# Kernel tuning notes

Measured on AMD Instinct MI355X. Metric: run time of the kernel, lower is better.

The kernel has to match this reference:

```python
import jax, jax.numpy as jnp
import numpy as np

D_MODEL = 1024
NUM_HEADS = 16
HEAD_DIM = D_MODEL // NUM_HEADS


def setup_inputs() -> dict:
    key = jax.random.key(0)
    ks = jax.random.split(key, 9)
    B, S = 2, 2048
    s = 1.0 / np.sqrt(D_MODEL)
    inp = {
        "x": jax.random.normal(ks[0], (B, S, D_MODEL), dtype=jnp.float32),
        "Wq": jax.random.normal(ks[1], (D_MODEL, D_MODEL), dtype=jnp.float32) * s,
        "bq": jnp.zeros((D_MODEL,), dtype=jnp.float32),
        "Wk": jax.random.normal(ks[2], (D_MODEL, D_MODEL), dtype=jnp.float32) * s,
        "bk": jnp.zeros((D_MODEL,), dtype=jnp.float32),
        "Wv": jax.random.normal(ks[3], (D_MODEL, D_MODEL), dtype=jnp.float32) * s,
        "bv": jnp.zeros((D_MODEL,), dtype=jnp.float32),
        "Wo": jax.random.normal(ks[4], (D_MODEL, D_MODEL), dtype=jnp.float32) * s,
        "bo": jnpp if False else jnp.zeros((D_MODEL,), dtype=jnp.float32),
    }
    return inp


def reference(x, Wq, bq, Wk, bk, Wv, bv, Wo, bo):
    B, S, D = x.shape
    H, hd = NUM_HEADS, HEAD_DIM
    # QKV projections (Linear: x @ W^T + b), split into heads -> [B,H,S,hd]
    q = (x @ Wq.T + bq).reshape(B, S, H, hd).transpose(0, 2, 1, 3)
    k = (x @ Wk.T + bk).reshape(B, S, H, hd).transpose(0, 2, 1, 3)
    v = (x @ Wv.T + bv).reshape(B, S, H, hd).transpose(0, 2, 1, 3)
    # scores [B,H,S,S]
    scores = jnp.einsum('bhqd,bhkd->bhqk', q, k) / jnp.sqrt(jnp.float32(hd))
    p = jax.nn.softmax(scores, axis=-1)
    out = jnp.einsum('bhqk,bhkd->bhqd', p, v)  # [B,H,S,hd]
    out = out.transpose(0, 2, 1, 3).reshape(B, S, D)
    return out @ Wo.T + bo
```

## Files before the change

### kernel.cpp

```cpp
#include <hip/hip_runtime.h>
#include <hip/hip_bf16.h>
#include <math.h>

typedef __bf16 bf16;
typedef unsigned short u16;
typedef __bf16 bf16x8 __attribute__((ext_vector_type(8)));
typedef __bf16 bf16x4 __attribute__((ext_vector_type(4)));
typedef short  s16x4  __attribute__((ext_vector_type(4)));
typedef float  f32x4  __attribute__((ext_vector_type(4)));

#define D_MODEL 1024
#define NHEAD   16
#define HD      64
#define BATCH   2
#define SEQ     2048
#define MTOT    (BATCH*SEQ)

#define EXPSCALE 0.18033688011116016f

__device__ __forceinline__ void async16(const void* g, void* l) {
    __builtin_amdgcn_global_load_lds(
        (__attribute__((address_space(1))) unsigned int*)g,
        (__attribute__((address_space(3))) unsigned int*)l,
        16, 0, 0);
}

__device__ __forceinline__ f32x4 mfma16(s16x4 a, s16x4 b, f32x4 c) {
    return __builtin_amdgcn_mfma_f32_16x16x16bf16_1k(a, b, c, 0, 0, 0);
}

__global__ __launch_bounds__(256) void cast_kernel(
    const float* __restrict__ x,
    const float* __restrict__ wq, const float* __restrict__ wk,
    const float* __restrict__ wv, const float* __restrict__ wo,
    bf16* __restrict__ xb, bf16* __restrict__ wqb, bf16* __restrict__ wkb,
    bf16* __restrict__ wvb, bf16* __restrict__ wob)
{
    const int z = blockIdx.y;
    const float* src;
    bf16* dst;
    int n;
    if (z == 0)      { src = x;  dst = xb;  n = MTOT * D_MODEL; }
    else if (z == 1) { src = wq; dst = wqb; n = D_MODEL * D_MODEL; }
    else if (z == 2) { src = wk; dst = wkb; n = D_MODEL * D_MODEL; }
    else if (z == 3) { src = wv; dst = wvb; n = D_MODEL * D_MODEL; }
    else             { src = wo; dst = wob; n = D_MODEL * D_MODEL; }

    int i = (blockIdx.x * 256 + threadIdx.x) * 8;
    if (i >= n) return;
    float4 a = *(const float4*)(src + i);
    float4 b = *(const float4*)(src + i + 4);
    bf16x8 o;
    o[0] = (bf16)a.x; o[1] = (bf16)a.y; o[2] = (bf16)a.z; o[3] = (bf16)a.w;
    o[4] = (bf16)b.x; o[5] = (bf16)b.y; o[6] = (bf16)b.z; o[7] = (bf16)b.w;
    *(bf16x8*)(dst + i) = o;
}

__device__ __forceinline__ void gemm_core(const bf16* __restrict__ A,
                                          const bf16* __restrict__ W,
                                          int m0, int n0,
                                          f32x4 acc[4][4],
                                          u16* lA, u16* lB)
{
    const int tid  = threadIdx.x;
    const int lane = tid & 63;
    const int wave = tid >> 6;
    const int wr   = wave >> 1;
    const int wc   = wave & 1;
    const int fr   = lane & 15;
    const int quad = lane >> 4;

    #pragma unroll
    for (int mi = 0; mi < 4; ++mi)
        #pragma unroll
        for (int ni = 0; ni < 4; ++ni)
            #pragma unroll
            for (int e = 0; e < 4; ++e)
                acc[mi][ni][e] = 0.0f;

    const int row = tid >> 3;
    const int ca  = ((tid & 7) ^ (row & 7)) * 8;
    const bf16* gA[4];
    const bf16* gB[4];
    u16 *sA[4], *sB[4];
    #pragma unroll
    for (int c = 0; c < 4; ++c) {
        int slot = tid + c * 256;
        int r    = row + c * 32;
        gA[c] = A + (size_t)(m0 + r) * 1024 + ca;
        gB[c] = W + (size_t)(n0 + r) * 1024 + ca;
        sA[c] = lA + (size_t)slot * 8;
        sB[c] = lB + (size_t)slot * 8;
    }

    for (int kt = 0; kt < 1024 / 64; ++kt) {
        __syncthreads();
        #pragma unroll
        for (int c = 0; c < 4; ++c) {
            async16(gA[c] + kt * 64, sA[c]);
            async16(gB[c] + kt * 64, sB[c]);
        }
        __syncthreads();

        #pragma unroll
        for (int ks = 0; ks < 2; ++ks) {
            const int sa = ((ks * 4 + quad) ^ (fr & 7)) * 8;
            bf16x8 af[4], bfm[4];
            #pragma unroll
            for (int mi = 0; mi < 4; ++mi)
                af[mi] = *(const bf16x8*)(lA + (wr * 64 + mi * 16 + fr) * 64 + sa);
            #pragma unroll
            for (int ni = 0; ni < 4; ++ni)
                bfm[ni] = *(const bf16x8*)(lB + (wc * 64 + ni * 16 + fr) * 64 + sa);

            #pragma unroll
            for (int mi = 0; mi < 4; ++mi)
                #pragma unroll
                for (int ni = 0; ni < 4; ++ni)
                    acc[mi][ni] = __builtin_amdgcn_mfma_f32_16x16x32_bf16(
                        af[mi], bfm[ni], acc[mi][ni], 0, 0, 0);
        }
    }
}

__global__ __launch_bounds__(256) void qkv_kernel(
    const bf16* __restrict__ x,
    const bf16* __restrict__ Wq, const bf16* __restrict__ Wk, const bf16* __restrict__ Wv,
    const float* __restrict__ bq, const float* __restrict__ bk, const float* __restrict__ bv,
    bf16* __restrict__ Q, bf16* __restrict__ K, bf16* __restrict__ Vt)
{
    __shared__ __align__(16) u16 lA[128 * 64];
    __shared__ __align__(16) u16 lB[128 * 64];

    const int z = blockIdx.z;
    int m0, n0;
    const bf16 *mA, *mB;
    const float* bias;
    if (z == 2) {
        mA = Wv; mB = x; bias = bv;
        m0 = blockIdx.y * 128;
        n0 = blockIdx.x * 128;
    } else {
        mA = x;  mB = (z == 0) ? Wq : Wk; bias = (z == 0) ? bq : bk;
        m0 = blockIdx.x * 128;
        n0 = blockIdx.y * 128;
    }

    f32x4 acc[4][4];
    gemm_core(mA, mB, m0, n0, acc, lA, lB);

    const int lane = threadIdx.x & 63;
    const int wave = threadIdx.x >> 6;
    const int wr = wave >> 1, wc = wave & 1;
    const int col = lane & 15, quad = lane >> 4;

    if (z == 2) {
        #pragma unroll
        for (int mi = 0; mi < 4; ++mi) {
            #pragma unroll
            for (int ni = 0; ni < 4; ++ni) {
                #pragma unroll
                for (int r = 0; r < 4; ++r) {
                    int f = m0 + wr * 64 + mi * 16 + quad * 4 + r;
                    int t = n0 + wc * 64 + ni * 16 + col;
                    float v = acc[mi][ni][r] + bias[f];
                    int b = t >> 11, s = t & 2047;
                    int h = f >> 6,  d = f & 63;
                    Vt[((size_t)(b * NHEAD + h) * HD + d) * SEQ + s] = (bf16)v;
                }
            }
        }
    } else {
        const float qs = (z == 0) ? EXPSCALE : 1.0f;
        bf16* o = (z == 0) ? Q : K;
        #pragma unroll
        for (int mi = 0; mi < 4; ++mi) {
            #pragma unroll
            for (int ni = 0; ni < 4; ++ni) {
                #pragma unroll
                for (int r = 0; r < 4; ++r) {
                    int m = m0 + wr * 64 + mi * 16 + quad * 4 + r;
                    int n = n0 + wc * 64 + ni * 16 + col;
                    float v = (acc[mi][ni][r] + bias[n]) * qs;
                    int b = m >> 11, s = m & 2047;
                    int h = n >> 6,  d = n & 63;
                    o[((size_t)(b * NHEAD + h) * SEQ + s) * HD + d] = (bf16)v;
                }
            }
        }
    }
}

__global__ __launch_bounds__(256, 2) void attn_kernel(
    const bf16* __restrict__ Q, const bf16* __restrict__ K,
    const bf16* __restrict__ Vt, bf16* __restrict__ O)
{
    __shared__ __align__(16) u16 lK[64 * 64];
    __shared__ __align__(16) u16 lV[64 * 64];

    const int tid  = threadIdx.x;
    const int lane = tid & 63;
    const int wave = tid >> 6;
    const int col  = lane & 15;
    const int quad = lane >> 4;
    const int bh   = blockIdx.x;
    const int q0   = blockIdx.y * 128;

    const bf16* Qh = Q  + (size_t)bh * SEQ * HD;
    const bf16* Kh = K  + (size_t)bh * SEQ * HD;
    const bf16* Vh = Vt + (size_t)bh * HD * SEQ;

    bf16x8 qf[2][2];
    #pragma unroll
    for (int qb = 0; qb < 2; ++qb)
        #pragma unroll
        for (int ks = 0; ks < 2; ++ks)
            qf[qb][ks] = *(const bf16x8*)(
                Qh + (size_t)(q0 + wave * 32 + qb * 16 + col) * HD + ks * 32 + quad * 8);

    f32x4 acc_o[2][4];
    #pragma unroll
    for (int qb = 0; qb < 2; ++qb)
        #pragma unroll
        for (int nd = 0; nd < 4; ++nd)
            #pragma unroll
            for (int e = 0; e < 4; ++e) acc_o[qb][nd][e] = 0.0f;
    float rs[2] = {0.0f, 0.0f};
    const f32x4 zero4 = {0.0f, 0.0f, 0.0f, 0.0f};

    const int r0 = tid >> 3;
    const int r1 = r0 + 32;
    const int g0 = (((tid & 7) ^ (r0 & 7))) * 8;
    const int g1 = (((tid & 7) ^ (r1 & 7))) * 8;
    const bf16* gK0 = Kh + (size_t)r0 * HD + g0;
    const bf16* gK1 = Kh + (size_t)r1 * HD + g1;
    const bf16* gV0 = Vh + (size_t)r0 * SEQ + g0;
    const bf16* gV1 = Vh + (size_t)r1 * SEQ + g1;
    u16* sK0 = lK + (size_t)tid * 8;
    u16* sK1 = lK + (size_t)(tid + 256) * 8;
    u16* sV0 = lV + (size_t)tid * 8;
    u16* sV1 = lV + (size_t)(tid + 256) * 8;

    for (int jt = 0; jt < SEQ / 64; ++jt) {
        __syncthreads();
        async16(gK0 + (size_t)jt * 64 * HD, sK0);
        async16(gK1 + (size_t)jt * 64 * HD, sK1);
        async16(gV0 + jt * 64, sV0);
        async16(gV1 + jt * 64, sV1);
        __syncthreads();

        f32x4 sc[2][4];
        #pragma unroll
        for (int nj = 0; nj < 4; ++nj) {
            bf16x8 kf0 = *(const bf16x8*)(
                lK + (nj * 16 + col) * 64 + ((0 + quad) ^ (col & 7)) * 8);
            sc[0][nj] = __builtin_amdgcn_mfma_f32_16x16x32_bf16(kf0, qf[0][0], zero4, 0, 0, 0);
            sc[1][nj] = __builtin_amdgcn_mfma_f32_16x16x32_bf16(kf0, qf[1][0], zero4, 0, 0, 0);
        }
        #pragma unroll
        for (int nj = 0; nj < 4; ++nj) {
            bf16x8 kf1 = *(const bf16x8*)(
                lK + (nj * 16 + col) * 64 + ((4 + quad) ^ (col & 7)) * 8);
            sc[0][nj] = __builtin_amdgcn_mfma_f32_16x16x32_bf16(kf1, qf[0][1], sc[0][nj], 0, 0, 0);
            sc[1][nj] = __builtin_amdgcn_mfma_f32_16x16x32_bf16(kf1, qf[1][1], sc[1][nj], 0, 0, 0);
        }

        s16x4 pb[2][4];
        #pragma unroll
        for (int qb = 0; qb < 2; ++qb) {
            #pragma unroll
            for (int nj = 0; nj < 4; ++nj) {
                float p0 = __builtin_amdgcn_exp2f(sc[qb][nj][0]);
                float p1 = __builtin_amdgcn_exp2f(sc[qb][nj][1]);
                float p2 = __builtin_amdgcn_exp2f(sc[qb][nj][2]);
                float p3 = __builtin_amdgcn_exp2f(sc[qb][nj][3]);
                rs[qb] += (p0 + p1) + (p2 + p3);
                bf16x4 t;
                t[0] = (bf16)p0; t[1] = (bf16)p1; t[2] = (bf16)p2; t[3] = (bf16)p3;
                pb[qb][nj] = __builtin_bit_cast(s16x4, t);
            }
        }

        #pragma unroll
        for (int nj = 0; nj < 4; ++nj) {
            #pragma unroll
            for (int nd = 0; nd < 4; ++nd) {
                int row = nd * 16 + col;
                int jb  = (2 * nj + (quad >> 1)) ^ (row & 7);
                s16x4 vb = *(const s16x4*)(lV + row * 64 + jb * 8 + (quad & 1) * 4);
                acc_o[0][nd] = mfma16(pb[0][nj], vb, acc_o[0][nd]);
                acc_o[1][nd] = mfma16(pb[1][nj], vb, acc_o[1][nd]);
            }
        }
    }

    const int b = bh >> 4, h = bh & 15;
    #pragma unroll
    for (int qb = 0; qb < 2; ++qb) {
        float v = rs[qb];
        v += __shfl_xor(v, 16);
        v += __shfl_xor(v, 32);
        float inv = 1.0f / v;
        float invr[4];
        #pragma unroll
        for (int r = 0; r < 4; ++r)
            invr[r] = __shfl(inv, quad * 4 + r);
        #pragma unroll
        for (int nd = 0; nd < 4; ++nd) {
            #pragma unroll
            for (int r = 0; r < 4; ++r) {
                int srow = q0 + wave * 32 + qb * 16 + quad * 4 + r;
                int d    = nd * 16 + col;
                float o  = acc_o[qb][nd][r] * invr[r];
                O[((size_t)(b * SEQ + srow)) * D_MODEL + h * HD + d] = (bf16)o;
            }
        }
    }
}

__global__ __launch_bounds__(256) void oproj_kernel(
    const bf16* __restrict__ A, const bf16* __restrict__ Wo,
    const float* __restrict__ bo, float* __restrict__ out)
{
    __shared__ __align__(16) u16 lA[128 * 64];
    __shared__ __align__(16) u16 lB[64 * 64];

    const int m0 = blockIdx.x * 128;
    const int n0 = blockIdx.y * 64;

    const int tid  = threadIdx.x;
    const int lane = tid & 63;
    const int wave = tid >> 6;
    const int wr   = wave >> 1;
    const int wc   = wave & 1;
    const int fr   = lane & 15;
    const int quad = lane >> 4;

    f32x4 acc[4][2];
    #pragma unroll
    for (int mi = 0; mi < 4; ++mi)
        #pragma unroll
        for (int ni = 0; ni < 2; ++ni)
            #pragma unroll
            for (int e = 0; e < 4; ++e)
                acc[mi][ni][e] = 0.0f;

    const int row = tid >> 3;
    const int ca  = ((tid & 7) ^ (row & 7)) * 8;
    const bf16* gA[4];
    u16* sA[4];
    #pragma unroll
    for (int c = 0; c < 4; ++c) {
        int slot = tid + c * 256;
        gA[c] = A + (size_t)(m0 + row + c * 32) * 1024 + ca;
        sA[c] = lA + (size_t)slot * 8;
    }
    const bf16* gB[2];
    u16* sB[2];
    #pragma unroll
    for (int c = 0; c < 2; ++c) {
        int slot = tid + c * 256;
        gB[c] = Wo + (size_t)(n0 + row + c * 32) * 1024 + ca;
        sB[c] = lB + (size_t)slot * 8;
    }

    for (int kt = 0; kt < 1024 / 64; ++kt) {
        __syncthreads();
        #pragma unroll
        for (int c = 0; c < 4; ++c) async16(gA[c] + kt * 64, sA[c]);
        #pragma unroll
        for (int c = 0; c < 2; ++c) async16(gB[c] + kt * 64, sB[c]);
        __syncthreads();

        #pragma unroll
        for (int ks = 0; ks < 2; ++ks) {
            const int sa = ((ks * 4 + quad) ^ (fr & 7)) * 8;
            bf16x8 af[4], bfm[2];
            #pragma unroll
            for (int mi = 0; mi < 4; ++mi)
                af[mi] = *(const bf16x8*)(lA + (wr * 64 + mi * 16 + fr) * 64 + sa);
            #pragma unroll
            for (int ni = 0; ni < 2; ++ni)
                bfm[ni] = *(const bf16x8*)(lB + (wc * 32 + ni * 16 + fr) * 64 + sa);

            #pragma unroll
            for (int mi = 0; mi < 4; ++mi)
                #pragma unroll
                for (int ni = 0; ni < 2; ++ni)
                    acc[mi][ni] = __builtin_amdgcn_mfma_f32_16x16x32_bf16(
                        af[mi], bfm[ni], acc[mi][ni], 0, 0, 0);
        }
    }

    const int col = fr;
    #pragma unroll
    for (int mi = 0; mi < 4; ++mi) {
        #pragma unroll
        for (int ni = 0; ni < 2; ++ni) {
            #pragma unroll
            for (int r = 0; r < 4; ++r) {
                int m = m0 + wr * 64 + mi * 16 + quad * 4 + r;
                int n = n0 + wc * 32 + ni * 16 + col;
                out[(size_t)m * D_MODEL + n] = acc[mi][ni][r] + bo[n];
            }
        }
    }
}

extern "C" void kernel_launch(void* const* d_in, const int* in_sizes, int n_in,
                              void* d_out, int out_size, void* d_ws, size_t ws_size,
                              hipStream_t stream)
{
    const float* x  = (const float*)d_in[0];
    const float* Wq = (const float*)d_in[1];
    const float* bq = (const float*)d_in[2];
    const float* Wk = (const float*)d_in[3];
    const float* bk = (const float*)d_in[4];
    const float* Wv = (const float*)d_in[5];
    const float* bv = (const float*)d_in[6];
    const float* Wo = (const float*)d_in[7];
    const float* bo = (const float*)d_in[8];
    float* out = (float*)d_out;

    char* ws = (char*)d_ws;
    const size_t XSZ = (size_t)MTOT * D_MODEL * sizeof(bf16);
    const size_t WSZ = (size_t)D_MODEL * D_MODEL * sizeof(bf16);
    bf16* wqb = (bf16*)(ws);
    bf16* wkb = (bf16*)(ws + WSZ);
    bf16* wvb = (bf16*)(ws + 2 * WSZ);
    bf16* wob = (bf16*)(ws + 3 * WSZ);
    bf16* xb  = (bf16*)(ws + 4 * WSZ);
    bf16* Qb  = (bf16*)(ws + 4 * WSZ + XSZ);
    bf16* Kb  = (bf16*)(ws + 4 * WSZ + 2 * XSZ);
    bf16* Vt  = (bf16*)(ws + 4 * WSZ + 3 * XSZ);
    bf16* At  = (bf16*)(ws + 4 * WSZ + 4 * XSZ);

    cast_kernel<<<dim3((MTOT * D_MODEL) / (256 * 8), 5), 256, 0, stream>>>(
        x, Wq, Wk, Wv, Wo, xb, wqb, wkb, wvb, wob);

    qkv_kernel<<<dim3(32, 8, 3), 256, 0, stream>>>(
        xb, wqb, wkb, wvb, bq, bk, bv, Qb, Kb, Vt);

    attn_kernel<<<dim3(BATCH * NHEAD, SEQ / 128), 256, 0, stream>>>(Qb, Kb, Vt, At);

    oproj_kernel<<<dim3(MTOT / 128, D_MODEL / 64), 256, 0, stream>>>(At, wob, bo, out);
}
```

Before: 192.1 us.

## Double-buffer K/V tiles in attention kernel to overlap loads with MFMA

After: 195.2 us. Within noise of the previous version (+1.6%).

```diff
diff --git a/kernel.cpp b/kernel.cpp
--- a/kernel.cpp
+++ b/kernel.cpp
@@ -195,8 +195,8 @@
     const bf16* __restrict__ Q, const bf16* __restrict__ K,
     const bf16* __restrict__ Vt, bf16* __restrict__ O)
 {
-    __shared__ __align__(16) u16 lK[64 * 64];
-    __shared__ __align__(16) u16 lV[64 * 64];
+    __shared__ __align__(16) u16 lK[2][64 * 64];
+    __shared__ __align__(16) u16 lV[2][64 * 64];
 
     const int tid  = threadIdx.x;
     const int lane = tid & 63;
@@ -236,31 +236,41 @@
     const bf16* gK1 = Kh + (size_t)r1 * HD + g1;
     const bf16* gV0 = Vh + (size_t)r0 * SEQ + g0;
     const bf16* gV1 = Vh + (size_t)r1 * SEQ + g1;
-    u16* sK0 = lK + (size_t)tid * 8;
-    u16* sK1 = lK + (size_t)(tid + 256) * 8;
-    u16* sV0 = lV + (size_t)tid * 8;
-    u16* sV1 = lV + (size_t)(tid + 256) * 8;
-
+    const int so0 = tid * 8;
+    const int so1 = (tid + 256) * 8;
+
+    async16(gK0, lK[0] + so0);
+    async16(gK1, lK[0] + so1);
+    async16(gV0, lV[0] + so0);
+    async16(gV1, lV[0] + so1);
+
+    int cur = 0;
     for (int jt = 0; jt < SEQ / 64; ++jt) {
         __syncthreads();
-        async16(gK0 + (size_t)jt * 64 * HD, sK0);
-        async16(gK1 + (size_t)jt * 64 * HD, sK1);
-        async16(gV0 + jt * 64, sV0);
-        async16(gV1 + jt * 64, sV1);
-        __syncthreads();
+
+        if (jt + 1 < SEQ / 64) {
+            const int nx = cur ^ 1;
+            async16(gK0 + (size_t)(jt + 1) * 64 * HD, lK[nx] + so0);
+            async16(gK1 + (size_t)(jt + 1) * 64 * HD, lK[nx] + so1);
+            async16(gV0 + (jt + 1) * 64, lV[nx] + so0);
+            async16(gV1 + (jt + 1) * 64, lV[nx] + so1);
+        }
+
+        const u16* K_ = lK[cur];
+        const u16* V_ = lV[cur];
 
         f32x4 sc[2][4];
         #pragma unroll
         for (int nj = 0; nj < 4; ++nj) {
             bf16x8 kf0 = *(const bf16x8*)(
-                lK + (nj * 16 + col) * 64 + ((0 + quad) ^ (col & 7)) * 8);
+                K_ + (nj * 16 + col) * 64 + ((0 + quad) ^ (col & 7)) * 8);
             sc[0][nj] = __builtin_amdgcn_mfma_f32_16x16x32_bf16(kf0, qf[0][0], zero4, 0, 0, 0);
             sc[1][nj] = __builtin_amdgcn_mfma_f32_16x16x32_bf16(kf0, qf[1][0], zero4, 0, 0, 0);
         }
         #pragma unroll
         for (int nj = 0; nj < 4; ++nj) {
             bf16x8 kf1 = *(const bf16x8*)(
-                lK + (nj * 16 + col) * 64 + ((4 + quad) ^ (col & 7)) * 8);
+                K_ + (nj * 16 + col) * 64 + ((4 + quad) ^ (col & 7)) * 8);
             sc[0][nj] = __builtin_amdgcn_mfma_f32_16x16x32_bf16(kf1, qf[0][1], sc[0][nj], 0, 0, 0);
             sc[1][nj] = __builtin_amdgcn_mfma_f32_16x16x32_bf16(kf1, qf[1][1], sc[1][nj], 0, 0, 0);
         }
@@ -287,11 +297,13 @@
             for (int nd = 0; nd < 4; ++nd) {
                 int row = nd * 16 + col;
                 int jb  = (2 * nj + (quad >> 1)) ^ (row & 7);
-                s16x4 vb = *(const s16x4*)(lV + row * 64 + jb * 8 + (quad & 1) * 4);
+                s16x4 vb = *(const s16x4*)(V_ + row * 64 + jb * 8 + (quad & 1) * 4);
                 acc_o[0][nd] = mfma16(pb[0][nj], vb, acc_o[0][nd]);
                 acc_o[1][nd] = mfma16(pb[1][nj], vb, acc_o[1][nd]);
             }
         }
+
+        cur ^= 1;
     }
 
     const int b = bh >> 4, h = bh & 15;
```

## Software-pipeline attention loop with double-buffered K and triple-buffered V

Applied to the files above, without the earlier changes.

Result: no change. 188.4 us (-1.9%).

```diff
diff --git a/kernel.cpp b/kernel.cpp
--- a/kernel.cpp
+++ b/kernel.cpp
@@ -195,8 +195,11 @@
     const bf16* __restrict__ Q, const bf16* __restrict__ K,
     const bf16* __restrict__ Vt, bf16* __restrict__ O)
 {
-    __shared__ __align__(16) u16 lK[64 * 64];
-    __shared__ __align__(16) u16 lV[64 * 64];
+    __shared__ __align__(16) u16 lK0[64 * 64];
+    __shared__ __align__(16) u16 lK1[64 * 64];
+    __shared__ __align__(16) u16 lV0[64 * 64];
+    __shared__ __align__(16) u16 lV1[64 * 64];
+    __shared__ __align__(16) u16 lV2[64 * 64];
 
     const int tid  = threadIdx.x;
     const int lane = tid & 63;
@@ -205,6 +208,7 @@
     const int quad = lane >> 4;
     const int bh   = blockIdx.x;
     const int q0   = blockIdx.y * 128;
+    const int NT   = SEQ / 64;
 
     const bf16* Qh = Q  + (size_t)bh * SEQ * HD;
     const bf16* Kh = K  + (size_t)bh * SEQ * HD;
@@ -236,61 +240,99 @@
     const bf16* gK1 = Kh + (size_t)r1 * HD + g1;
     const bf16* gV0 = Vh + (size_t)r0 * SEQ + g0;
     const bf16* gV1 = Vh + (size_t)r1 * SEQ + g1;
-    u16* sK0 = lK + (size_t)tid * 8;
-    u16* sK1 = lK + (size_t)(tid + 256) * 8;
-    u16* sV0 = lV + (size_t)tid * 8;
-    u16* sV1 = lV + (size_t)(tid + 256) * 8;
-
-    for (int jt = 0; jt < SEQ / 64; ++jt) {
+    const int so0 = tid * 8;
+    const int so1 = (tid + 256) * 8;
+
+    async16(gK0, lK0 + so0);
+    async16(gK1, lK0 + so1);
+    async16(gV0, lV0 + so0);
+    async16(gV1, lV0 + so1);
+
+    u16 *kRd = lK0, *kSt = lK1;
+    u16 *vRd = lV2, *vCur = lV0, *vSt = lV1;
+
+    s16x4 pb0[4], pb1[4];
+
+    for (int jt = 0; jt < NT; ++jt) {
         __syncthreads();
-        async16(gK0 + (size_t)jt * 64 * HD, sK0);
-        async16(gK1 + (size_t)jt * 64 * HD, sK1);
-        async16(gV0 + jt * 64, sV0);
-        async16(gV1 + jt * 64, sV1);
-        __syncthreads();
-
-        f32x4 sc[2][4];
+
+        if (jt + 1 < NT) {
+            async16(gK0 + (size_t)(jt + 1) * 64 * HD, kSt + so0);
+            async16(gK1 + (size_t)(jt + 1) * 64 * HD, kSt + so1);
+            async16(gV0 + (jt + 1) * 64, vSt + so0);
+            async16(gV1 + (jt + 1) * 64, vSt + so1);
+        }
+
+        __builtin_amdgcn_s_setprio(1);
+
+        f32x4 sc0[4], sc1[4];
         #pragma unroll
         for (int nj = 0; nj < 4; ++nj) {
             bf16x8 kf0 = *(const bf16x8*)(
-                lK + (nj * 16 + col) * 64 + ((0 + quad) ^ (col & 7)) * 8);
-            sc[0][nj] = __builtin_amdgcn_mfma_f32_16x16x32_bf16(kf0, qf[0][0], zero4, 0, 0, 0);
-            sc[1][nj] = __builtin_amdgcn_mfma_f32_16x16x32_bf16(kf0, qf[1][0], zero4, 0, 0, 0);
+                kRd + (nj * 16 + col) * 64 + ((0 + quad) ^ (col & 7)) * 8);
+            sc0[nj] = __builtin_amdgcn_mfma_f32_16x16x32_bf16(kf0, qf[0][0], zero4, 0, 0, 0);
+            sc1[nj] = __builtin_amdgcn_mfma_f32_16x16x32_bf16(kf0, qf[1][0], zero4, 0, 0, 0);
         }
         #pragma unroll
         for (int nj = 0; nj < 4; ++nj) {
             bf16x8 kf1 = *(const bf16x8*)(
-                lK + (nj * 16 + col) * 64 + ((4 + quad) ^ (col & 7)) * 8);
-            sc[0][nj] = __builtin_amdgcn_mfma_f32_16x16x32_bf16(kf1, qf[0][1], sc[0][nj], 0, 0, 0);
-            sc[1][nj] = __builtin_amdgcn_mfma_f32_16x16x32_bf16(kf1, qf[1][1], sc[1][nj], 0, 0, 0);
-        }
-
-        s16x4 pb[2][4];
-        #pragma unroll
-        for (int qb = 0; qb < 2; ++qb) {
+                kRd + (nj * 16 + col) * 64 + ((4 + quad) ^ (col & 7)) * 8);
+            sc0[nj] = __builtin_amdgcn_mfma_f32_16x16x32_bf16(kf1, qf[0][1], sc0[nj], 0, 0, 0);
+            sc1[nj] = __builtin_amdgcn_mfma_f32_16x16x32_bf16(kf1, qf[1][1], sc1[nj], 0, 0, 0);
+        }
+
+        if (jt > 0) {
             #pragma unroll
             for (int nj = 0; nj < 4; ++nj) {
-                float p0 = __builtin_amdgcn_exp2f(sc[qb][nj][0]);
-                float p1 = __builtin_amdgcn_exp2f(sc[qb][nj][1]);
-                float p2 = __builtin_amdgcn_exp2f(sc[qb][nj][2]);
-                float p3 = __builtin_amdgcn_exp2f(sc[qb][nj][3]);
-                rs[qb] += (p0 + p1) + (p2 + p3);
-                bf16x4 t;
-                t[0] = (bf16)p0; t[1] = (bf16)p1; t[2] = (bf16)p2; t[3] = (bf16)p3;
-                pb[qb][nj] = __builtin_bit_cast(s16x4, t);
+                #pragma unroll
+                for (int nd = 0; nd < 4; ++nd) {
+                    int row = nd * 16 + col;
+                    int jb  = (2 * nj + (quad >> 1)) ^ (row & 7);
+                    s16x4 vb = *(const s16x4*)(vRd + row * 64 + jb * 8 + (quad & 1) * 4);
+                    acc_o[0][nd] = mfma16(pb0[nj], vb, acc_o[0][nd]);
+                    acc_o[1][nd] = mfma16(pb1[nj], vb, acc_o[1][nd]);
+                }
             }
         }
 
+        __builtin_amdgcn_s_setprio(0);
+
         #pragma unroll
         for (int nj = 0; nj < 4; ++nj) {
-            #pragma unroll
-            for (int nd = 0; nd < 4; ++nd) {
-                int row = nd * 16 + col;
-                int jb  = (2 * nj + (quad >> 1)) ^ (row & 7);
-                s16x4 vb = *(const s16x4*)(lV + row * 64 + jb * 8 + (quad & 1) * 4);
-                acc_o[0][nd] = mfma16(pb[0][nj], vb, acc_o[0][nd]);
-                acc_o[1][nd] = mfma16(pb[1][nj], vb, acc_o[1][nd]);
-            }
+            float p0 = __builtin_amdgcn_exp2f(sc0[nj][0]);
+            float p1 = __builtin_amdgcn_exp2f(sc0[nj][1]);
+            float p2 = __builtin_amdgcn_exp2f(sc0[nj][2]);
+            float p3 = __builtin_amdgcn_exp2f(sc0[nj][3]);
+            rs[0] += (p0 + p1) + (p2 + p3);
+            bf16x4 t;
+            t[0] = (bf16)p0; t[1] = (bf16)p1; t[2] = (bf16)p2; t[3] = (bf16)p3;
+            pb0[nj] = __builtin_bit_cast(s16x4, t);
+        }
+        #pragma unroll
+        for (int nj = 0; nj < 4; ++nj) {
+            float p0 = __builtin_amdgcn_exp2f(sc1[nj][0]);
+            float p1 = __builtin_amdgcn_exp2f(sc1[nj][1]);
+            float p2 = __builtin_amdgcn_exp2f(sc1[nj][2]);
+            float p3 = __builtin_amdgcn_exp2f(sc1[nj][3]);
+            rs[1] += (p0 + p1) + (p2 + p3);
+            bf16x4 t;
+            t[0] = (bf16)p0; t[1] = (bf16)p1; t[2] = (bf16)p2; t[3] = (bf16)p3;
+            pb1[nj] = __builtin_bit_cast(s16x4, t);
+        }
+
+        u16* tk = kRd; kRd = kSt; kSt = tk;
+        u16* tv = vRd; vRd = vCur; vCur = vSt; vSt = tv;
+    }
+
+    #pragma unroll
+    for (int nj = 0; nj < 4; ++nj) {
+        #pragma unroll
+        for (int nd = 0; nd < 4; ++nd) {
+            int row = nd * 16 + col;
+            int jb  = (2 * nj + (quad >> 1)) ^ (row & 7);
+            s16x4 vb = *(const s16x4*)(vRd + row * 64 + jb * 8 + (quad & 1) * 4);
+            acc_o[0][nd] = mfma16(pb0[nj], vb, acc_o[0][nd]);
+            acc_o[1][nd] = mfma16(pb1[nj], vb, acc_o[1][nd]);
         }
     }
 
```
